# Optimization experiments

Hardware: AMD Instinct MI355X
Metric: run time of the kernel (lower is better)

Reference implementation:

```python
import jax, jax.numpy as jnp
import numpy as np

HEADS = 16
KV_HEADS = 4
DIM_HEAD = 128
DIM = 2048
ROPE_BASE = 10000.0


def rotate_half(t):
    t1, t2 = jnp.split(t, 2, axis=-1)
    return jnp.concatenate((-t2, t1), axis=-1)


def apply_rotary(t, cos, sin):
    # t: [b, h, n, d]; cos/sin: [n, d]
    return t * cos + rotate_half(t) * sin


def setup_inputs() -> dict:
    key = jax.random.key(0)
    ks = jax.random.split(key, 6)
    b, n = 4, 1024
    s = 1.0 / np.sqrt(DIM)
    x = jax.random.normal(ks[0], (b, n, DIM), dtype=jnp.float32)
    Wq = jax.random.normal(ks[1], (DIM, HEADS * DIM_HEAD), dtype=jnp.float32) * s
    Wk = jax.random.normal(ks[2], (DIM, KV_HEADS * DIM_HEAD), dtype=jnp.float32) * s
    Wv = jax.random.normal(ks[3], (DIM, KV_HEADS * DIM_HEAD), dtype=jnp.float32) * s
    Wo = jax.random.normal(ks[4], (HEADS * DIM_HEAD, DIM), dtype=jnp.float32) * s
    head_scale = 1.0 + 0.02 * jax.random.normal(ks[5], (1, HEADS, 1, 1), dtype=jnp.float32)
    return {"x": x, "Wq": Wq, "Wk": Wk, "Wv": Wv, "Wo": Wo, "head_scale": head_scale}


def reference(x, Wq, Wk, Wv, Wo, head_scale):
    b, n, _ = x.shape
    # projections
    q = (x @ Wq).reshape(b, n, HEADS, DIM_HEAD).transpose(0, 2, 1, 3)      # b h n d
    k = (x @ Wk).reshape(b, n, KV_HEADS, DIM_HEAD).transpose(0, 2, 1, 3)   # b kv n d
    v = (x @ Wv).reshape(b, n, KV_HEADS, DIM_HEAD).transpose(0, 2, 1, 3)
    # rotary embeddings
    inv_freq = 1.0 / (ROPE_BASE ** (jnp.arange(0, DIM_HEAD, 2, dtype=jnp.float32) / DIM_HEAD))
    freqs = jnp.arange(n, dtype=jnp.float32)[:, None] * inv_freq[None, :]  # n, d/2
    emb = jnp.concatenate((freqs, freqs), axis=-1)                          # n, d
    cos, sin = jnp.cos(emb), jnp.sin(emb)
    q = apply_rotary(q, cos, sin)
    k = apply_rotary(k, cos, sin)
    # GQA: expand kv heads to query heads
    rep = HEADS // KV_HEADS
    k = jnp.repeat(k, rep, axis=1)
    v = jnp.repeat(v, rep, axis=1)
    # attention with causal mask
    scale = 1.0 / jnp.sqrt(jnp.array(DIM_HEAD, dtype=x.dtype))
    scores = jnp.einsum('bhid,bhjd->bhij', q, k) * scale
    causal = jnp.tril(jnp.ones((n, n), dtype=bool))
    scores = jnp.where(causal, scores, jnp.finfo(scores.dtype).min)
    attn = jax.nn.softmax(scores, axis=-1)
    out = jnp.einsum('bhij,bhjd->bhid', attn, v)
    out = out * head_scale                                                  # learned per-head scale
    out = out.transpose(0, 2, 1, 3).reshape(b, n, HEADS * DIM_HEAD)
    return out @ Wo
```

## Files before the change

### kernel.cpp

```cpp
#include <hip/hip_runtime.h>

typedef __attribute__((ext_vector_type(8))) short short8;
typedef __attribute__((ext_vector_type(8), may_alias)) short short8a;
typedef __attribute__((ext_vector_type(4))) short short4a_ __attribute__((may_alias));
typedef __attribute__((ext_vector_type(2), may_alias)) short short2a;
typedef __attribute__((ext_vector_type(4))) float float4_;
typedef __attribute__((ext_vector_type(4), may_alias)) float float4a;
typedef __attribute__((ext_vector_type(2), may_alias)) float float2a;

__device__ __forceinline__ float b2f(short h) {
  unsigned int u = ((unsigned int)(unsigned short)h) << 16;
  return __builtin_bit_cast(float, u);
}
__device__ __forceinline__ short f2b(float f) {
  unsigned int u = __builtin_bit_cast(unsigned int, f);
  u += 0x7fffu + ((u >> 16) & 1u);
  return (short)(unsigned short)(u >> 16);
}

#define GLOBAL_AS __attribute__((address_space(1)))
#define LDS_AS    __attribute__((address_space(3)))
__device__ __forceinline__ void async_copy16(void* lds, const void* g) {
  __builtin_amdgcn_global_load_lds((GLOBAL_AS const void*)g, (LDS_AS void*)lds, 16, 0, 0);
}

__global__ __launch_bounds__(256) void prep(const float* __restrict__ x,
                                            const float* __restrict__ Wq,
                                            const float* __restrict__ Wk,
                                            const float* __restrict__ Wv,
                                            const float* __restrict__ Wo,
                                            short* __restrict__ xb,
                                            short* __restrict__ wqkvt,
                                            short* __restrict__ wot,
                                            float* __restrict__ rtab) {
  __shared__ float tile[64][65];
  int bid = blockIdx.x;
  if (bid < 1536) {
    int k0 = (bid & 31) * 64, n0 = (bid >> 5) * 64;
    for (int idx = threadIdx.x; idx < 4096; idx += 256) {
      int r = idx >> 6, cc = idx & 63;
      int n = n0 + cc;
      float v;
      if (n < 2048)      v = Wq[(size_t)(k0 + r) * 2048 + n] * 0.08838834764831845f;
      else if (n < 2560) v = Wk[(size_t)(k0 + r) * 512 + (n - 2048)];
      else               v = Wv[(size_t)(k0 + r) * 512 + (n - 2560)];
      tile[r][cc] = v;
    }
    __syncthreads();
    for (int idx = threadIdx.x; idx < 4096; idx += 256) {
      int r = idx >> 6, cc = idx & 63;
      wqkvt[(size_t)(n0 + r) * 2048 + k0 + cc] = f2b(tile[cc][r]);
    }
  } else if (bid < 2560) {
    int t = bid - 1536;
    int k0 = (t & 31) * 64, n0 = (t >> 5) * 64;
    for (int idx = threadIdx.x; idx < 4096; idx += 256) {
      int r = idx >> 6, cc = idx & 63;
      tile[r][cc] = Wo[(size_t)(k0 + r) * 2048 + n0 + cc];
    }
    __syncthreads();
    for (int idx = threadIdx.x; idx < 4096; idx += 256) {
      int r = idx >> 6, cc = idx & 63;
      wot[(size_t)(n0 + r) * 2048 + k0 + cc] = f2b(tile[cc][r]);
    }
  } else if (bid < 10752) {
    int i = (bid - 2560) * 256 + threadIdx.x;
    float4a v = ((const float4a*)x)[i];
    short4a_ o;
    o.x = f2b(v.x); o.y = f2b(v.y); o.z = f2b(v.z); o.w = f2b(v.w);
    ((short4a_*)xb)[i] = o;
  } else {
    int idx = (bid - 10752) * 256 + threadIdx.x;
    int pos = idx >> 6, i = idx & 63;
    float inv = exp2f((float)i * -0.20762050593478f);
    float s, c;
    sincosf((float)pos * inv, &s, &c);
    float2a cs; cs.x = c; cs.y = s;
    ((float2a*)rtab)[idx] = cs;
  }
}

__global__ __launch_bounds__(256, 2)
void gemm_rope(const short* __restrict__ A, const short* __restrict__ B,
               short* __restrict__ Cb, const float* __restrict__ rtab,
               short* __restrict__ vt, int M, int N, int K) {
  __shared__ alignas(16) short lsm[16896];
  short* lA = lsm;
  short* lB = lsm + 8192;
  const int tid = threadIdx.x;
  const int wave = tid >> 6, lane = tid & 63;
  const int quad = lane >> 4, l16 = lane & 15;
  const int m0 = blockIdx.x * 128, n0 = blockIdx.y * 128;
  const int wm = (wave >> 1) * 64, wn = (wave & 1) * 64;
  float4_ acc[4][4];
#pragma unroll
  for (int i = 0; i < 4; i++)
#pragma unroll
    for (int j = 0; j < 4; j++) acc[i][j] = (float4_){0.f, 0.f, 0.f, 0.f};
  const int nK = K >> 6;
  const int srow = lane >> 3, slot = lane & 7;
  for (int kt = 0; kt < nK; ++kt) {
    __syncthreads();
#pragma unroll
    for (int cth = 0; cth < 4; ++cth) {
      int rb = wave * 32 + cth * 8;
      int r = rb + srow;
      int c = slot ^ (r & 7);
      async_copy16(&lA[rb * 64], A + (size_t)(m0 + r) * K + kt * 64 + c * 8);
      async_copy16(&lB[rb * 64], B + (size_t)(n0 + r) * K + kt * 64 + c * 8);
    }
    __syncthreads();
#pragma unroll
    for (int kc = 0; kc < 2; ++kc) {
      short8 af[4], bf[4];
      int cch = kc * 4 + quad;
#pragma unroll
      for (int mt = 0; mt < 4; ++mt) {
        int ar = wm + mt * 16 + l16;
        af[mt] = *(const short8a*)&lA[ar * 64 + (cch ^ (ar & 7)) * 8];
      }
#pragma unroll
      for (int nt = 0; nt < 4; ++nt) {
        int br = wn + nt * 16 + l16;
        bf[nt] = *(const short8a*)&lB[br * 64 + (cch ^ (br & 7)) * 8];
      }
#pragma unroll
      for (int mt = 0; mt < 4; ++mt)
#pragma unroll
        for (int nt = 0; nt < 4; ++nt)
          acc[mt][nt] = __builtin_amdgcn_mfma_f32_16x16x32_bf16(af[mt], bf[nt], acc[mt][nt], 0, 0, 0);
    }
  }
  const bool isRope = (n0 < 2560);
  __syncthreads();
  short* lC = lsm;
  const int posBase = m0 & 1023;
  float4a tv[16];
  if (isRope) {
#pragma unroll
    for (int it = 0; it < 16; ++it) {
      int idx = it * 256 + tid;
      int row = idx >> 5, c2 = (idx & 31) * 2;
      tv[it] = *(const float4a*)&rtab[((size_t)(posBase + row) * 64 + c2) * 2];
    }
  }
#pragma unroll
  for (int mt = 0; mt < 4; ++mt)
#pragma unroll
    for (int nt = 0; nt < 4; ++nt)
#pragma unroll
      for (int r = 0; r < 4; r++)
        lC[(wm + mt * 16 + quad * 4 + r) * 132 + wn + nt * 16 + l16] = f2b(acc[mt][nt][r]);
  __syncthreads();
  if (isRope) {
#pragma unroll
    for (int it = 0; it < 16; ++it) {
      int idx = it * 256 + tid;
      int row = idx >> 5;
      int c2 = (idx & 31) * 2;
      short2a t1 = *(const short2a*)&lC[row * 132 + c2];
      short2a t2 = *(const short2a*)&lC[row * 132 + c2 + 64];
      float t1a = b2f(t1.x), t1b = b2f(t1.y);
      float t2a = b2f(t2.x), t2b = b2f(t2.y);
      float4a t = tv[it];
      short2a o1, o2;
      o1.x = f2b(t1a * t.x - t2a * t.y); o1.y = f2b(t1b * t.z - t2b * t.w);
      o2.x = f2b(t2a * t.x + t1a * t.y); o2.y = f2b(t2b * t.z + t1b * t.w);
      size_t base = (size_t)(m0 + row) * N + n0;
      *(short2a*)&Cb[base + c2] = o1;
      *(short2a*)&Cb[base + c2 + 64] = o2;
    }
  } else {
    const int bkv = (m0 >> 10) * 4 + ((n0 - 2560) >> 7);
#pragma unroll
    for (int it = 0; it < 8; ++it) {
      int idx = it * 256 + tid;
      int d = idx >> 4, jc = idx & 15;
      short8 v;
#pragma unroll
      for (int k = 0; k < 8; ++k) v[k] = lC[(jc * 8 + k) * 132 + d];
      *(short8a*)&vt[((size_t)(bkv * 128 + d)) * 1024 + posBase + jc * 8] = v;
    }
  }
}

#define FENCE() __builtin_amdgcn_sched_barrier(0)

template <int N_>
__device__ __forceinline__ void waitv() {
  if constexpr (N_ == 6)      asm volatile("s_waitcnt vmcnt(6)" ::: "memory");
  else if constexpr (N_ == 3) asm volatile("s_waitcnt vmcnt(3)" ::: "memory");
  else                        asm volatile("s_waitcnt vmcnt(0)" ::: "memory");
}

#define STG2(P_, KH_, T_, PART_)                                                   \
  do { if ((T_) < nK) {                                                            \
    const size_t co_ = (size_t)(T_) * 64 + (KH_) * 32;                             \
    if ((PART_) == 0) {                                                            \
      async_copy16(&lsm[(P_) * 24576 + (KH_) * 4096 + wave * 512], Asrc + co_);    \
      async_copy16(&lsm[(P_) * 24576 + 8192 + (KH_) * 8192 + wave * 512],          \
                   Bsrc + co_);                                                    \
    } else {                                                                       \
      async_copy16(&lsm[(P_) * 24576 + 8192 + (KH_) * 8192 + 4096 + wave * 512],   \
                   Bsrc + 128 * (size_t)K + co_);                                  \
    }                                                                              \
  } } while (0)

#define WAITG2(G_)                                                                 \
  do { int rem_ = 2 * nK - 2 - (G_);                                               \
    if (rem_ >= 2) waitv<6>();                                                     \
    else if (rem_ == 1) waitv<3>();                                                \
    else waitv<0>(); } while (0)

#define PHASED2(P_, KK_, STAGE0, STAGE1, ENDW)                                     \
  {                                                                                \
    short8 af[4];                                                                  \
    _Pragma("unroll") for (int mi = 0; mi < 4; ++mi)                               \
      af[mi] = *(const short8a*)&lsm[(P_) * 24576 + (KK_) * 4096 + aoff[mi]];      \
    short8 bf[4];                                                                  \
    _Pragma("unroll") for (int ni = 0; ni < 4; ++ni)                               \
      bf[ni] = *(const short8a*)&lsm[(P_) * 24576 + 8192 + (KK_) * 8192 +          \
                                     boff[ni]];                                    \
    STAGE0; STAGE1;                                                                \
    FENCE();                                                                       \
    __builtin_amdgcn_s_barrier();                                                  \
    FENCE();                                                                       \
    __builtin_amdgcn_s_setprio(1);                                                 \
    _Pragma("unroll") for (int mi = 0; mi < 4; ++mi)                               \
      _Pragma("unroll") for (int ni = 0; ni < 4; ++ni)                             \
        acc[mi][ni] = __builtin_amdgcn_mfma_f32_16x16x32_bf16(                     \
            af[mi], bf[ni], acc[mi][ni], 0, 0, 0);                                 \
    __builtin_amdgcn_s_setprio(0);                                                 \
    FENCE();                                                                       \
    ENDW;                                                                          \
    __builtin_amdgcn_s_barrier();                                                  \
    FENCE();                                                                       \
  }

__global__ __launch_bounds__(512, 2)
void gemm_out(const short* __restrict__ A, const short* __restrict__ B,
              float* __restrict__ Cf, int M, int N, int K) {
  __shared__ alignas(16) short lsm[49152];
  const int tid = threadIdx.x;
  const int wave = tid >> 6, lane = tid & 63;
  const int quad = lane >> 4, l16 = lane & 15;
  const int m0 = blockIdx.x * 128, n0 = blockIdx.y * 256;
  const int wm = (wave >> 2) * 64, wn = (wave & 3) * 64;
  const int nK = K >> 6;

  int aoff[4], boff[4];
#pragma unroll
  for (int j = 0; j < 4; ++j) {
    int r = wm + j * 16 + l16;
    aoff[j] = r * 32 + (quad ^ ((r >> 1) & 3)) * 8;
  }
#pragma unroll
  for (int ni = 0; ni < 4; ++ni) {
    int r = wn + ni * 16 + l16;
    boff[ni] = r * 32 + (quad ^ ((r >> 1) & 3)) * 8;
  }
  const int r0 = tid >> 2;
  const int qq = (tid & 3) ^ ((r0 >> 1) & 3);
  const short* Asrc = A + (size_t)(m0 + r0) * K + qq * 8;
  const short* Bsrc = B + (size_t)(n0 + r0) * K + qq * 8;

  float4_ acc[4][4];
#pragma unroll
  for (int i = 0; i < 4; i++)
#pragma unroll
    for (int j = 0; j < 4; j++) acc[i][j] = (float4_){0.f, 0.f, 0.f, 0.f};

  STG2(0, 0, 0, 0); STG2(0, 0, 0, 1);
  STG2(0, 1, 0, 0); STG2(0, 1, 0, 1);
  STG2(1, 0, 1, 0); STG2(1, 0, 1, 1);
  FENCE();
  waitv<6>();
  __builtin_amdgcn_s_barrier();
  FENCE();

  for (int t = 0; t < nK; t += 2) {
    PHASED2(0, 0, STG2(1, 1, t + 1, 0), STG2(1, 1, t + 1, 1), WAITG2(2 * t));
    PHASED2(0, 1, STG2(0, 0, t + 2, 0), STG2(0, 0, t + 2, 1), WAITG2(2 * t + 1));
    PHASED2(1, 0, STG2(0, 1, t + 2, 0), STG2(0, 1, t + 2, 1), WAITG2(2 * t + 2));
    PHASED2(1, 1, STG2(1, 0, t + 3, 0), STG2(1, 0, t + 3, 1), WAITG2(2 * t + 3));
  }

#pragma unroll
  for (int mt = 0; mt < 4; ++mt)
#pragma unroll
    for (int ni = 0; ni < 4; ++ni) {
      int row = m0 + wm + mt * 16 + quad * 4;
      int col = n0 + wn + ni * 16 + l16;
      float4_ v = acc[mt][ni];
#pragma unroll
      for (int r = 0; r < 4; r++) Cf[(size_t)(row + r) * N + col] = v[r];
    }
}

__global__ __launch_bounds__(256, 2)
void flash(const short* __restrict__ qkv, const short* __restrict__ vt,
           const float* __restrict__ head_scale, short* __restrict__ attn) {
  __shared__ alignas(16) short lK[64 * 128];
  __shared__ alignas(16) short lV[128 * 64];
  __shared__ alignas(16) short lP[4][32 * 72];
  const int tid = threadIdx.x, wave = tid >> 6, lane = tid & 63;
  const int quad = lane >> 4, l16 = lane & 15;
  const int bh = blockIdx.x, b = bh >> 4, h = bh & 15, kv = h >> 2;
  const int qt = 7 - blockIdx.y;
  const int base_w = qt * 128 + wave * 32;
  short8 qf[2][4];
#pragma unroll
  for (int g = 0; g < 2; g++) {
    int qrow = base_w + g * 16 + l16;
    const short* qp = qkv + (size_t)(b * 1024 + qrow) * 3072 + h * 128;
#pragma unroll
    for (int kc = 0; kc < 4; kc++) qf[g][kc] = *(const short8a*)(qp + kc * 32 + quad * 8);
  }
  float4_ O[2][8];
#pragma unroll
  for (int g = 0; g < 2; g++)
#pragma unroll
    for (int i = 0; i < 8; i++) O[g][i] = (float4_){0.f, 0.f, 0.f, 0.f};
  float rsacc[2][4] = {{0.f, 0.f, 0.f, 0.f}, {0.f, 0.f, 0.f, 0.f}};
  const size_t kbase = (size_t)(b * 1024) * 3072 + 2048 + kv * 128;
  const size_t vbase = (size_t)((b * 4 + kv) * 128) * 1024;
  const int slot16 = lane & 15, rr4 = lane >> 4;
  const int slot8 = lane & 7, dr8 = lane >> 3;
  const int nkt = 2 * qt + 2;
  for (int kt = 0; kt < nkt; ++kt) {
    __syncthreads();
#pragma unroll
    for (int cc = 0; cc < 4; ++cc) {
      int rb = wave * 16 + cc * 4;
      int r = rb + rr4;
      int c = slot16 ^ (r & 15);
      async_copy16(&lK[rb * 128], qkv + kbase + (size_t)(kt * 64 + r) * 3072 + c * 8);
    }
#pragma unroll
    for (int cc = 0; cc < 4; ++cc) {
      int db = wave * 32 + cc * 8;
      int d = db + dr8;
      int c = slot8 ^ (d & 7);
      async_copy16(&lV[db * 64], vt + vbase + (size_t)d * 1024 + kt * 64 + c * 8);
    }
    __syncthreads();
    if (kt * 64 > base_w + 31) continue;
    float4_ S[2][4];
#pragma unroll
    for (int st = 0; st < 4; ++st) {
      float4_ s0 = (float4_){0.f, 0.f, 0.f, 0.f}, s1 = s0;
      int kr = st * 16 + l16;
#pragma unroll
      for (int kc = 0; kc < 4; ++kc) {
        int c = kc * 4 + quad;
        short8 kf = *(const short8a*)&lK[kr * 128 + (c ^ (kr & 15)) * 8];
        s0 = __builtin_amdgcn_mfma_f32_16x16x32_bf16(qf[0][kc], kf, s0, 0, 0, 0);
        s1 = __builtin_amdgcn_mfma_f32_16x16x32_bf16(qf[1][kc], kf, s1, 0, 0, 0);
      }
      S[0][st] = s0; S[1][st] = s1;
    }
#pragma unroll
    for (int g = 0; g < 2; g++) {
      int gbase = base_w + g * 16;
      if (kt * 64 + 63 > gbase) {
#pragma unroll
        for (int st = 0; st < 4; ++st)
#pragma unroll
          for (int r = 0; r < 4; r++)
            if (kt * 64 + st * 16 + l16 > gbase + quad * 4 + r) S[g][st][r] = -1e30f;
      }
#pragma unroll
      for (int st = 0; st < 4; ++st)
#pragma unroll
        for (int r = 0; r < 4; r++) {
          float pv = __expf(S[g][st][r]);
          rsacc[g][r] += pv;
          lP[wave][(g * 16 + quad * 4 + r) * 72 + st * 16 + l16] = f2b(pv);
        }
    }
    short8 pf[2][2];
#pragma unroll
    for (int g = 0; g < 2; g++)
#pragma unroll
      for (int kc2 = 0; kc2 < 2; kc2++)
        pf[g][kc2] = *(const short8a*)&lP[wave][(g * 16 + l16) * 72 + kc2 * 32 + quad * 8];
#pragma unroll
    for (int dt = 0; dt < 8; ++dt) {
      int d = dt * 16 + l16;
#pragma unroll
      for (int kc2 = 0; kc2 < 2; kc2++) {
        int c = kc2 * 4 + quad;
        short8 vf = *(const short8a*)&lV[d * 64 + (c ^ (d & 7)) * 8];
        O[0][dt] = __builtin_amdgcn_mfma_f32_16x16x32_bf16(pf[0][kc2], vf, O[0][dt], 0, 0, 0);
        O[1][dt] = __builtin_amdgcn_mfma_f32_16x16x32_bf16(pf[1][kc2], vf, O[1][dt], 0, 0, 0);
      }
    }
  }
  float hs = head_scale[h];
#pragma unroll
  for (int g = 0; g < 2; g++) {
    float l_i[4];
#pragma unroll
    for (int r = 0; r < 4; r++) {
      float rs = rsacc[g][r];
#pragma unroll
      for (int off = 8; off; off >>= 1) rs += __shfl_xor(rs, off, 64);
      l_i[r] = rs;
    }
    int qrow = base_w + g * 16 + quad * 4;
#pragma unroll
    for (int dt = 0; dt < 8; ++dt) {
      int col = h * 128 + dt * 16 + l16;
#pragma unroll
      for (int r = 0; r < 4; r++) {
        float o = O[g][dt][r] * (hs / l_i[r]);
        attn[(size_t)(b * 1024 + qrow + r) * 2048 + col] = f2b(o);
      }
    }
  }
}

extern "C" void kernel_launch(void* const* d_in, const int* in_sizes, int n_in,
                              void* d_out, int out_size, void* d_ws, size_t ws_size,
                              hipStream_t stream) {
  const float* x  = (const float*)d_in[0];
  const float* Wq = (const float*)d_in[1];
  const float* Wk = (const float*)d_in[2];
  const float* Wv = (const float*)d_in[3];
  const float* Wo = (const float*)d_in[4];
  const float* hs = (const float*)d_in[5];
  float* out = (float*)d_out;
  char* ws = (char*)d_ws;
  short* xb    = (short*)(ws);
  short* wqkvt = (short*)(ws + 16777216);
  short* wot   = (short*)(ws + 29360128);
  short* qkv   = (short*)(ws + 37748736);
  short* vt    = (short*)(ws + 62914560);
  short* attn  = xb;
  float* rtab  = out + 8257536;

  prep<<<11008, 256, 0, stream>>>(x, Wq, Wk, Wv, Wo, xb, wqkvt, wot, rtab);
  gemm_rope<<<dim3(32, 24), 256, 0, stream>>>(xb, wqkvt, qkv, rtab, vt, 4096, 3072, 2048);
  flash<<<dim3(64, 8), 256, 0, stream>>>(qkv, vt, hs, attn);
  gemm_out<<<dim3(32, 8), 512, 0, stream>>>(attn, wot, out, 4096, 2048, 2048);
}
```

Baseline: 252.0 us.

## Prefetch next K/V tile into registers while computing current attention tile

Replaces the per-iteration async global-to-LDS copies of K and V with a register-staged software pipeline. The next tile is loaded into registers before the current tile's QK^T, softmax and PV compute, then written to LDS after a barrier. This is meant to hide global load latency behind MFMA work instead of stalling on the copy each iteration. It costs extra VGPRs for staging, which may lower occupancy, and adds a second barrier pair per tile.

```diff
diff --git a/kernel.cpp b/kernel.cpp
--- a/kernel.cpp
+++ b/kernel.cpp
@@ -327,73 +327,88 @@
   const int slot16 = lane & 15, rr4 = lane >> 4;
   const int slot8 = lane & 7, dr8 = lane >> 3;
   const int nkt = 2 * qt + 2;
+
+  short8 kreg[4], vreg[4];
+#define LOADT(KT_)                                                              \
+  { _Pragma("unroll") for (int cc = 0; cc < 4; ++cc) {                          \
+      int r = wave * 16 + cc * 4 + rr4;                                         \
+      int c = slot16 ^ (r & 15);                                                \
+      kreg[cc] = *(const short8a*)(qkv + kbase +                                \
+                    (size_t)((KT_) * 64 + r) * 3072 + c * 8);                   \
+    }                                                                           \
+    _Pragma("unroll") for (int cc = 0; cc < 4; ++cc) {                          \
+      int d = wave * 32 + cc * 8 + dr8;                                         \
+      int c = slot8 ^ (d & 7);                                                  \
+      vreg[cc] = *(const short8a*)(vt + vbase + (size_t)d * 1024 +              \
+                    (KT_) * 64 + c * 8);                                        \
+    } }
+#define WRITET()                                                                \
+  { _Pragma("unroll") for (int cc = 0; cc < 4; ++cc)                            \
+      *(short8a*)&lK[(wave * 16 + cc * 4) * 128 + lane * 8] = kreg[cc];         \
+    _Pragma("unroll") for (int cc = 0; cc < 4; ++cc)                            \
+      *(short8a*)&lV[(wave * 32 + cc * 8) * 64 + lane * 8] = vreg[cc]; }
+
+  LOADT(0);
+  WRITET();
+  __syncthreads();
   for (int kt = 0; kt < nkt; ++kt) {
-    __syncthreads();
-#pragma unroll
-    for (int cc = 0; cc < 4; ++cc) {
-      int rb = wave * 16 + cc * 4;
-      int r = rb + rr4;
-      int c = slot16 ^ (r & 15);
-      async_copy16(&lK[rb * 128], qkv + kbase + (size_t)(kt * 64 + r) * 3072 + c * 8);
-    }
-#pragma unroll
-    for (int cc = 0; cc < 4; ++cc) {
-      int db = wave * 32 + cc * 8;
-      int d = db + dr8;
-      int c = slot8 ^ (d & 7);
-      async_copy16(&lV[db * 64], vt + vbase + (size_t)d * 1024 + kt * 64 + c * 8);
-    }
-    __syncthreads();
-    if (kt * 64 > base_w + 31) continue;
-    float4_ S[2][4];
-#pragma unroll
-    for (int st = 0; st < 4; ++st) {
-      float4_ s0 = (float4_){0.f, 0.f, 0.f, 0.f}, s1 = s0;
-      int kr = st * 16 + l16;
-#pragma unroll
-      for (int kc = 0; kc < 4; ++kc) {
-        int c = kc * 4 + quad;
-        short8 kf = *(const short8a*)&lK[kr * 128 + (c ^ (kr & 15)) * 8];
-        s0 = __builtin_amdgcn_mfma_f32_16x16x32_bf16(qf[0][kc], kf, s0, 0, 0, 0);
-        s1 = __builtin_amdgcn_mfma_f32_16x16x32_bf16(qf[1][kc], kf, s1, 0, 0, 0);
-      }
-      S[0][st] = s0; S[1][st] = s1;
-    }
-#pragma unroll
-    for (int g = 0; g < 2; g++) {
-      int gbase = base_w + g * 16;
-      if (kt * 64 + 63 > gbase) {
+    if (kt + 1 < nkt) LOADT(kt + 1);
+    if (kt * 64 <= base_w + 31) {
+      float4_ S[2][4];
+#pragma unroll
+      for (int st = 0; st < 4; ++st) {
+        float4_ s0 = (float4_){0.f, 0.f, 0.f, 0.f}, s1 = s0;
+        int kr = st * 16 + l16;
+#pragma unroll
+        for (int kc = 0; kc < 4; ++kc) {
+          int c = kc * 4 + quad;
+          short8 kf = *(const short8a*)&lK[kr * 128 + (c ^ (kr & 15)) * 8];
+          s0 = __builtin_amdgcn_mfma_f32_16x16x32_bf16(qf[0][kc], kf, s0, 0, 0, 0);
+          s1 = __builtin_amdgcn_mfma_f32_16x16x32_bf16(qf[1][kc], kf, s1, 0, 0, 0);
+        }
+        S[0][st] = s0; S[1][st] = s1;
+      }
+#pragma unroll
+      for (int g = 0; g < 2; g++) {
+        int gbase = base_w + g * 16;
+        if (kt * 64 + 63 > gbase) {
+#pragma unroll
+          for (int st = 0; st < 4; ++st)
+#pragma unroll
+            for (int r = 0; r < 4; r++)
+              if (kt * 64 + st * 16 + l16 > gbase + quad * 4 + r) S[g][st][r] = -1e30f;
+        }
 #pragma unroll
         for (int st = 0; st < 4; ++st)
 #pragma unroll
-          for (int r = 0; r < 4; r++)
-            if (kt * 64 + st * 16 + l16 > gbase + quad * 4 + r) S[g][st][r] = -1e30f;
-      }
-#pragma unroll
-      for (int st = 0; st < 4; ++st)
-#pragma unroll
-        for (int r = 0; r < 4; r++) {
-          float pv = __expf(S[g][st][r]);
-          rsacc[g][r] += pv;
-          lP[wave][(g * 16 + quad * 4 + r) * 72 + st * 16 + l16] = f2b(pv);
+          for (int r = 0; r < 4; r++) {
+            float pv = __expf(S[g][st][r]);
+            rsacc[g][r] += pv;
+            lP[wave][(g * 16 + quad * 4 + r) * 72 + st * 16 + l16] = f2b(pv);
+          }
+      }
+      short8 pf[2][2];
+#pragma unroll
+      for (int g = 0; g < 2; g++)
+#pragma unroll
+        for (int kc2 = 0; kc2 < 2; kc2++)
+          pf[g][kc2] = *(const short8a*)&lP[wave][(g * 16 + l16) * 72 + kc2 * 32 + quad * 8];
+#pragma unroll
+      for (int dt = 0; dt < 8; ++dt) {
+        int d = dt * 16 + l16;
+#pragma unroll
+        for (int kc2 = 0; kc2 < 2; kc2++) {
+          int c = kc2 * 4 + quad;
+          short8 vf = *(const short8a*)&lV[d * 64 + (c ^ (d & 7)) * 8];
+          O[0][dt] = __builtin_amdgcn_mfma_f32_16x16x32_bf16(pf[0][kc2], vf, O[0][dt], 0, 0, 0);
+          O[1][dt] = __builtin_amdgcn_mfma_f32_16x16x32_bf16(pf[1][kc2], vf, O[1][dt], 0, 0, 0);
         }
-    }
-    short8 pf[2][2];
-#pragma unroll
-    for (int g = 0; g < 2; g++)
-#pragma unroll
-      for (int kc2 = 0; kc2 < 2; kc2++)
-        pf[g][kc2] = *(const short8a*)&lP[wave][(g * 16 + l16) * 72 + kc2 * 32 + quad * 8];
-#pragma unroll
-    for (int dt = 0; dt < 8; ++dt) {
-      int d = dt * 16 + l16;
-#pragma unroll
-      for (int kc2 = 0; kc2 < 2; kc2++) {
-        int c = kc2 * 4 + quad;
-        short8 vf = *(const short8a*)&lV[d * 64 + (c ^ (d & 7)) * 8];
-        O[0][dt] = __builtin_amdgcn_mfma_f32_16x16x32_bf16(pf[0][kc2], vf, O[0][dt], 0, 0, 0);
-        O[1][dt] = __builtin_amdgcn_mfma_f32_16x16x32_bf16(pf[1][kc2], vf, O[1][dt], 0, 0, 0);
-      }
+      }
+    }
+    if (kt + 1 < nkt) {
+      __syncthreads();
+      WRITET();
+      __syncthreads();
     }
   }
   float hs = head_scale[h];
@@ -418,6 +433,8 @@
       }
     }
   }
+#undef LOADT
+#undef WRITET
 }
 
 extern "C" void kernel_launch(void* const* d_in, const int* in_sizes, int n_in,
```

After: 250.2 us, median of 2. About the same (-0.7%).
